# Optimization experiments

Hardware: AMD Instinct MI355X
Metric: run time of the kernel (lower is better)

Reference implementation:

```python
import jax, jax.numpy as jnp
import numpy as np

HK, DK, HV, DV = 16, 128, 32, 128
VE = (HV // HK) * DV  # 256
CHUNK = 64
KSZ = 4
EPS = 1e-12


def l2_normalize(x):
    sq = jnp.sum(x * x, axis=-1, keepdims=True)
    return x * jax.lax.rsqrt(sq + EPS)


def causal_dwconv_silu(x_bct, w, b):
    # x_bct: [B, C, T]; w: [C, 1, K]; b: [C]; causal depthwise conv then SiLU
    C = x_bct.shape[1]
    y = jax.lax.conv_general_dilated(
        x_bct, w, window_strides=(1,), padding=[(KSZ - 1, 0)],
        dimension_numbers=('NCH', 'OIH', 'NCH'), feature_group_count=C)
    return jax.nn.silu(y + b[None, :, None])


def setup_inputs() -> dict:
    key = jax.random.key(0)
    ks = jax.random.split(key, 12)
    B, T, H = 2, 2048, 2048
    s = 0.02
    return {
        'x': jax.random.normal(ks[0], (B, T, H), jnp.float32),
        'state': jnp.zeros((B, HK, DK, VE), jnp.float32),
        'Wq': jax.random.normal(ks[1], (HK * DK, H), jnp.float32) * s,
        'Wk': jax.random.normal(ks[2], (HK * DK, H), jnp.float32) * s,
        'Wv': jax.random.normal(ks[3], (HV * DV, H), jnp.float32) * s,
        'Wo': jax.random.normal(ks[4], (H, HV * DV), jnp.float32) * s,
        'Wa': jax.random.normal(ks[5], (HK, H), jnp.float32) * s,
        'Wb': jax.random.normal(ks[6], (HK, H), jnp.float32) * s,
        'qcW': jax.random.normal(ks[7], (HK * DK, 1, KSZ), jnp.float32) * 0.3,
        'qcB': jnp.zeros((HK * DK,), jnp.float32),
        'kcW': jax.random.normal(ks[8], (HK * DK, 1, KSZ), jnp.float32) * 0.3,
        'kcB': jnp.zeros((HK * DK,), jnp.float32),
        'vcW': jax.random.normal(ks[9], (HV * DV, 1, KSZ), jnp.float32) * 0.3,
        'vcB': jnp.zeros((HV * DV,), jnp.float32),
    }


def _forward(x, state, Wq, Wk, Wv, Wo, Wa, Wb, qcW, qcB, kcW, kcB, vcW, vcB):
    B, T, H = x.shape
    Cn = CHUNK
    # T is a multiple of CHUNK here (no padding needed)
    nc = T // Cn
    x_bct = jnp.transpose(x, (0, 2, 1))  # [B, H, T]
    # 1x1-conv projections == channelwise linear
    q = causal_dwconv_silu(jnp.einsum('qh,bht->bqt', Wq, x_bct), qcW, qcB)
    k = causal_dwconv_silu(jnp.einsum('qh,bht->bqt', Wk, x_bct), kcW, kcB)
    v = causal_dwconv_silu(jnp.einsum('vh,bht->bvt', Wv, x_bct), vcW, vcB)
    alpha = jax.nn.sigmoid(jnp.einsum('gh,bht->bgt', Wa, x_bct))  # [B,HK,T]
    beta = jax.nn.sigmoid(jnp.einsum('gh,bht->bgt', Wb, x_bct))

    q = jnp.transpose(q, (0, 2, 1)).reshape(B, T, HK, DK)
    k = jnp.transpose(k, (0, 2, 1)).reshape(B, T, HK, DK)
    # regroup value heads by key head: [B,T,HV,DV] -> [B,T,HK,VE]
    v = jnp.transpose(v, (0, 2, 1)).reshape(B, T, HK, VE)
    alpha = jnp.transpose(alpha, (0, 2, 1))  # [B,T,HK]
    beta = jnp.transpose(beta, (0, 2, 1))

    q = l2_normalize(q)
    k = l2_normalize(k)

    # time-major, chunked: [nc, Cn, B, HK, ...]
    def tmchunk(a):
        a = jnp.moveaxis(a, 1, 0)  # [T, B, ...]
        return a.reshape((nc, Cn) + a.shape[1:])

    qc, kc, vc, ac, bc = map(tmchunk, (q, k, v, alpha, beta))

    def step(s, inp):
        qt, kt, vt, at, bt = inp  # qt/kt [B,HK,DK], vt [B,HK,VE], at/bt [B,HK]
        s = s * at[..., None, None]
        retrieved = jnp.einsum('bhkv,bhk->bhv', s, kt)
        err = vt - retrieved
        s = s + bt[..., None, None] * (kt[..., :, None] * err[..., None, :])
        ot = jnp.einsum('bhkv,bhk->bhv', s, qt)
        return s, ot

    @jax.checkpoint
    def chunk_step(s, ch):
        return jax.lax.scan(step, s, ch)

    state, outs = jax.lax.scan(chunk_step, state, (qc, kc, vc, ac, bc))
    # outs: [nc, Cn, B, HK, VE] -> [B, T, HV*DV]
    out = outs.reshape(T, B, HK * VE)
    out = jnp.moveaxis(out, 0, 1)
    out = jnp.einsum('btv,ov->bto', out, Wo)
    return out, state


def reference(x, state, Wq, Wk, Wv, Wo, Wa, Wb, qcW, qcB, kcW, kcB, vcW, vcB):
    return _forward(x, state, Wq, Wk, Wv, Wo, Wa, Wb, qcW, qcB, kcW, kcB, vcW, vcB)
```

## Files before the change

kernel.cpp:

```cpp
#include <hip/hip_runtime.h>
#include <hip/hip_bf16.h>

typedef __attribute__((ext_vector_type(8))) __bf16 bf16x8;
typedef __attribute__((ext_vector_type(8))) short short8;
typedef __attribute__((ext_vector_type(4))) float floatx4;
using u16 = unsigned short;

#define GLOBAL_AS __attribute__((address_space(1)))
#define LDS_AS    __attribute__((address_space(3)))

__device__ __forceinline__ float b2f(u16 u) {
    union { unsigned int i; float f; } v; v.i = ((unsigned int)u) << 16; return v.f;
}
__device__ __forceinline__ u16 f2b(float f) {
    __hip_bfloat16 h = __float2bfloat16(f);
    return __builtin_bit_cast(u16, h);
}
__device__ __forceinline__ float ldf(const void* p, long i, bool isf32) {
    return isf32 ? ((const float*)p)[i] : b2f(((const u16*)p)[i]);
}
__device__ __forceinline__ void gload_lds16(const void* g, void* l) {
    __builtin_amdgcn_global_load_lds((const GLOBAL_AS unsigned int*)g,
                                     (LDS_AS unsigned int*)l, 16, 0, 0);
}
__device__ __forceinline__ float red8(float x) {
    int xi, yi;
    xi = __builtin_bit_cast(int, x);
    yi = __builtin_amdgcn_update_dpp(xi, xi, 0xB1, 0xF, 0xF, false);
    x += __builtin_bit_cast(float, yi);
    xi = __builtin_bit_cast(int, x);
    yi = __builtin_amdgcn_update_dpp(xi, xi, 0x4E, 0xF, 0xF, false);
    x += __builtin_bit_cast(float, yi);
    xi = __builtin_bit_cast(int, x);
    yi = __builtin_amdgcn_update_dpp(xi, xi, 0x141, 0xF, 0xF, false);
    x += __builtin_bit_cast(float, yi);
    return x;
}
__device__ __forceinline__ void unpack2(int d, float& lo, float& hi) {
    lo = __builtin_bit_cast(float, (int)((unsigned)d << 16));
    hi = __builtin_bit_cast(float, d & 0xffff0000);
}
__device__ __forceinline__ void unpack8(int4 d, float* f) {
    unpack2(d.x, f[0], f[1]); unpack2(d.y, f[2], f[3]);
    unpack2(d.z, f[4], f[5]); unpack2(d.w, f[6], f[7]);
}

__global__ void detect_dtype(const unsigned int* __restrict__ x, int* __restrict__ flag) {
    const int lane = threadIdx.x;
    int sane = 0;
    for (int i = lane; i < 256; i += 64) {
        const unsigned e = (x[i] >> 23) & 0xFF;
        sane += (e >= 100 && e <= 140) ? 1 : 0;
    }
#pragma unroll
    for (int m = 1; m < 64; m <<= 1) sane += __shfl_xor(sane, m, 64);
    if (lane == 0) *flag = (sane >= 128) ? 1 : 0;
}

__global__ __launch_bounds__(256) void cvt_bf16(
    const void* __restrict__ in, u16* __restrict__ out, long n, const int* __restrict__ flag) {
    const bool f32 = (*flag != 0);
    const long i = ((long)blockIdx.x * 256 + threadIdx.x) * 8;
    if (i >= n) return;
    if (f32) {
        const float* p = (const float*)in + i;
        floatx4 a = *(const floatx4*)p, b = *(const floatx4*)(p + 4);
        short8 o;
        o[0] = (short)f2b(a[0]); o[1] = (short)f2b(a[1]);
        o[2] = (short)f2b(a[2]); o[3] = (short)f2b(a[3]);
        o[4] = (short)f2b(b[0]); o[5] = (short)f2b(b[1]);
        o[6] = (short)f2b(b[2]); o[7] = (short)f2b(b[3]);
        *(short8*)(out + i) = o;
    } else {
        *(int4*)(out + i) = *(const int4*)((const u16*)in + i);
    }
}

__global__ __launch_bounds__(256) void gemm_bt128(
    const u16* __restrict__ A, const u16* __restrict__ B, void* __restrict__ C,
    int M, int N, int K, int cmode, const int* __restrict__ flag) {
    const bool c32 = (cmode == 1) || (cmode == 2 && *flag != 0);
    __shared__ __align__(16) u16 As[128 * 32];
    __shared__ __align__(16) u16 Bs[128 * 32];
    const int tid = threadIdx.x, lane = tid & 63, wave = tid >> 6;
    const int bm = blockIdx.y * 128, bn = blockIdx.x * 128;
    const int wm = (wave >> 1) * 64, wn = (wave & 1) * 64;
    const int fr = lane & 15, fq = lane >> 4;
    floatx4 acc[4][4] = {};

    const int srow = tid >> 2, scol = (tid & 3) * 8;
    const long abase = (long)(bm + srow) * K + scol;
    const long bbase = (long)(bn + srow) * K + scol;
    char* lA = (char*)As + (tid & ~63) * 16;
    char* lB = (char*)Bs + (tid & ~63) * 16;

    for (int k0 = 0; k0 < K; k0 += 32) {
        __syncthreads();
        gload_lds16(A + abase + k0, lA);
        gload_lds16(A + abase + (long)64 * K + k0, lA + 4096);
        gload_lds16(B + bbase + k0, lB);
        gload_lds16(B + bbase + (long)64 * K + k0, lB + 4096);
        __syncthreads();
        bf16x8 af[4], bf[4];
#pragma unroll
        for (int i = 0; i < 4; i++) {
            af[i] = __builtin_bit_cast(bf16x8, *(const short8*)&As[(wm + i * 16 + fr) * 32 + fq * 8]);
            bf[i] = __builtin_bit_cast(bf16x8, *(const short8*)&Bs[(wn + i * 16 + fr) * 32 + fq * 8]);
        }
#pragma unroll
        for (int mi = 0; mi < 4; mi++)
#pragma unroll
            for (int ni = 0; ni < 4; ni++)
                acc[mi][ni] = __builtin_amdgcn_mfma_f32_16x16x32_bf16(
                    af[mi], bf[ni], acc[mi][ni], 0, 0, 0);
    }
#pragma unroll
    for (int mi = 0; mi < 4; mi++)
#pragma unroll
        for (int ni = 0; ni < 4; ni++)
#pragma unroll
            for (int r = 0; r < 4; r++) {
                const int m = bm + wm + mi * 16 + fq * 4 + r;
                const int n = bn + wn + ni * 16 + fr;
                const float val = acc[mi][ni][r];
                const long ci = (long)m * N + n;
                if (c32) ((float*)C)[ci] = val;
                else ((u16*)C)[ci] = f2b(val);
            }
}

__global__ __launch_bounds__(256) void ab_gemm(
    const u16* __restrict__ xb, const u16* __restrict__ wab,
    float* __restrict__ alphaT, float* __restrict__ betaT) {
    __shared__ __align__(16) u16 As[64 * 64];
    __shared__ __align__(16) u16 Bs[32 * 64];
    const int tid = threadIdx.x, lane = tid & 63, wave = tid >> 6;
    const int bm = blockIdx.x * 64;
    const int fr = lane & 15, fq = lane >> 4;
    floatx4 acc[2] = {};

    const int srow = tid >> 3, scol = (tid & 7) * 8;
    char* lA = (char*)As + (tid & ~63) * 16;
    char* lB = (char*)Bs + (tid & ~63) * 16;

    for (int k0 = 0; k0 < 2048; k0 += 64) {
        __syncthreads();
        gload_lds16(xb + (long)(bm + srow) * 2048 + k0 + scol, lA);
        gload_lds16(xb + (long)(bm + 32 + srow) * 2048 + k0 + scol, lA + 4096);
        gload_lds16(wab + (long)srow * 2048 + k0 + scol, lB);
        __syncthreads();
#pragma unroll
        for (int ks = 0; ks < 2; ks++) {
            bf16x8 af = __builtin_bit_cast(bf16x8,
                *(const short8*)&As[(wave * 16 + fr) * 64 + ks * 32 + fq * 8]);
#pragma unroll
            for (int nt = 0; nt < 2; nt++) {
                bf16x8 bf = __builtin_bit_cast(bf16x8,
                    *(const short8*)&Bs[(nt * 16 + fr) * 64 + ks * 32 + fq * 8]);
                acc[nt] = __builtin_amdgcn_mfma_f32_16x16x32_bf16(af, bf, acc[nt], 0, 0, 0);
            }
        }
    }
#pragma unroll
    for (int nt = 0; nt < 2; nt++)
#pragma unroll
        for (int r = 0; r < 4; r++) {
            const int m = bm + wave * 16 + fq * 4 + r;
            const int n = nt * 16 + fr;
            const int b = m >> 11, t = m & 2047;
            const float s = 1.f / (1.f + __expf(-acc[nt][r]));
            if (n < 16) alphaT[((long)b * 16 + n) * 2048 + t] = s;
            else betaT[((long)b * 16 + (n - 16)) * 2048 + t] = s;
        }
}

__global__ __launch_bounds__(256) void conv_silu_norm(
    const u16* __restrict__ pre, const void* __restrict__ cw,
    const void* __restrict__ cb, u16* __restrict__ out, const int* __restrict__ flag) {
    const bool f32 = (*flag != 0);
    const int bt = blockIdx.x;
    const int t = bt & 2047;
    const int tid = threadIdx.x;
    const int c0 = tid * 8;
    float y[8];
    float ss = 0.f;
#pragma unroll
    for (int j = 0; j < 8; j++) {
        const int c = c0 + j;
        float acc = ldf(cb, c, f32);
#pragma unroll
        for (int i = 0; i < 4; i++) {
            if (t - 3 + i >= 0)
                acc += ldf(cw, c * 4 + i, f32) * b2f(pre[(long)(bt - 3 + i) * 2048 + c]);
        }
        const float s = acc / (1.f + __expf(-acc));
        y[j] = s;
        ss += s * s;
    }
#pragma unroll
    for (int m = 1; m < 16; m <<= 1) ss += __shfl_xor(ss, m, 64);
    const float inv = rsqrtf(ss + 1e-12f);
#pragma unroll
    for (int j = 0; j < 8; j++) out[(long)bt * 2048 + c0 + j] = f2b(y[j] * inv);
}

__global__ __launch_bounds__(256) void conv_silu_v(
    const u16* __restrict__ pre, const void* __restrict__ cw,
    const void* __restrict__ cb, u16* __restrict__ out, const int* __restrict__ flag) {
    const bool f32 = (*flag != 0);
    const int bt = blockIdx.x;
    const int t = bt & 2047;
    const int tid = threadIdx.x;
    const int c0 = tid * 16;
#pragma unroll
    for (int j = 0; j < 16; j++) {
        const int c = c0 + j;
        float acc = ldf(cb, c, f32);
#pragma unroll
        for (int i = 0; i < 4; i++) {
            if (t - 3 + i >= 0)
                acc += ldf(cw, c * 4 + i, f32) * b2f(pre[(long)(bt - 3 + i) * 4096 + c]);
        }
        out[(long)bt * 4096 + c] = f2b(acc / (1.f + __expf(-acc)));
    }
}

__global__ __launch_bounds__(256) void recurrence_kernel(
    const u16* __restrict__ qn, const u16* __restrict__ kn,
    const u16* __restrict__ vn, const float* __restrict__ alphaT,
    const float* __restrict__ betaT, const void* __restrict__ state_in,
    u16* __restrict__ outs, void* __restrict__ d_out, const int* __restrict__ flag) {
    const bool f32 = (*flag != 0);
    const int blk = blockIdx.x;
    const int vb = blk & 7, h = (blk >> 3) & 15, b = blk >> 7;
    const int tid = threadIdx.x, lane = tid & 63, wave = tid >> 6;
    const int kg = lane & 7, vq = lane >> 3;
    const int vloc = wave * 8 + vq;
    const int vglob = vb * 32 + vloc;

    float S[16];
    const long stbase = ((long)(b * 16 + h) * 128 + kg * 16) * 256 + vglob;
#pragma unroll
    for (int j = 0; j < 16; j++) S[j] = ldf(state_in, stbase + (long)j * 256, f32);

    __shared__ __align__(16) u16 kbuf[16 * 128];
    __shared__ __align__(16) u16 qbuf[16 * 128];
    __shared__ __align__(16) u16 vbuf[16 * 32];

    const long abase = (long)(b * 16 + h) * 2048;
    const int srow = tid >> 4, scol = (tid & 15) * 8;
    char* lK = (char*)kbuf + (tid & ~63) * 16;
    char* lQ = (char*)qbuf + (tid & ~63) * 16;

    for (int c = 0; c < 128; ++c) {
        const int t0 = c * 16;
        const float aw = alphaT[abase + t0 + (lane & 15)];
        const float bw = betaT[abase + t0 + (lane & 15)];
        __syncthreads();
        const long gkq = ((long)b * 2048 + t0 + srow) * 2048 + h * 128 + scol;
        gload_lds16(kn + gkq, lK);
        gload_lds16(qn + gkq, lQ);
        if (tid < 64) {
            const long gv = ((long)b * 2048 + t0 + (lane >> 2)) * 4096 + h * 256 + vb * 32 + (lane & 3) * 8;
            gload_lds16(vn + gv, (char*)vbuf);
        }
        __syncthreads();

        int4 kA = *(const int4*)(kbuf + kg * 16);
        int4 kB = *(const int4*)(kbuf + kg * 16 + 8);
        int4 qA = *(const int4*)(qbuf + kg * 16);
        int4 qB = *(const int4*)(qbuf + kg * 16 + 8);
        u16 vcur = vbuf[vloc];

#pragma unroll
        for (int tt = 0; tt < 16; ++tt) {
            int4 kA_n, kB_n, qA_n, qB_n;
            u16 v_n;
            if (tt < 15) {
                kA_n = *(const int4*)(kbuf + (tt + 1) * 128 + kg * 16);
                kB_n = *(const int4*)(kbuf + (tt + 1) * 128 + kg * 16 + 8);
                qA_n = *(const int4*)(qbuf + (tt + 1) * 128 + kg * 16);
                qB_n = *(const int4*)(qbuf + (tt + 1) * 128 + kg * 16 + 8);
                v_n  = vbuf[(tt + 1) * 32 + vloc];
            }
            const float a = __builtin_bit_cast(float,
                __builtin_amdgcn_readlane(__builtin_bit_cast(int, aw), tt));
            const float bb = __builtin_bit_cast(float,
                __builtin_amdgcn_readlane(__builtin_bit_cast(int, bw), tt));
            float kf[16], qf[16];
            unpack8(kA, kf);
            unpack8(kB, kf + 8);
            unpack8(qA, qf);
            unpack8(qB, qf + 8);
            float r0 = 0.f, r1 = 0.f;
#pragma unroll
            for (int j = 0; j < 8; j++) {
                r0 = fmaf(S[j], kf[j], r0);
                r1 = fmaf(S[8 + j], kf[8 + j], r1);
            }
            float r = red8(r0 + r1);
            const float vv = b2f(vcur);
            const float err = fmaf(-a, r, vv);
            const float cc = bb * err;
            float o0 = 0.f, o1 = 0.f;
#pragma unroll
            for (int j = 0; j < 8; j++) {
                S[j] = fmaf(cc, kf[j], a * S[j]);
                S[8 + j] = fmaf(cc, kf[8 + j], a * S[8 + j]);
                o0 = fmaf(S[j], qf[j], o0);
                o1 = fmaf(S[8 + j], qf[8 + j], o1);
            }
            const float o = red8(o0 + o1);
            if (kg == 0)
                outs[((long)b * 2048 + t0 + tt) * 4096 + h * 256 + vglob] = f2b(o);
            if (tt < 15) { kA = kA_n; kB = kB_n; qA = qA_n; qB = qB_n; vcur = v_n; }
        }
    }
#pragma unroll
    for (int j = 0; j < 16; j++) {
        const long idx = 8388608L + stbase + (long)j * 256;
        if (f32) ((float*)d_out)[idx] = S[j];
        else ((u16*)d_out)[idx] = f2b(S[j]);
    }
}

extern "C" void kernel_launch(void* const* d_in, const int* in_sizes, int n_in,
                              void* d_out, int out_size, void* d_ws, size_t ws_size,
                              hipStream_t stream) {
    const void* x   = d_in[0];
    const void* st0 = d_in[1];
    const void* Wq  = d_in[2];
    const void* Wk  = d_in[3];
    const void* Wv  = d_in[4];
    const void* Wo  = d_in[5];
    const void* Wa  = d_in[6];
    const void* Wb  = d_in[7];
    const void* qcW = d_in[8];
    const void* qcB = d_in[9];
    const void* kcW = d_in[10];
    const void* kcB = d_in[11];
    const void* vcW = d_in[12];
    const void* vcB = d_in[13];

    const int M = 4096;
    const long MB = 1024L * 1024L;
    char* w = (char*)d_ws;
    int*   flag   = (int*)w;
    float* alphaT = (float*)(w + 1024);
    float* betaT  = (float*)(w + 1024 + 262144);
    u16*   wab    = (u16*)(w + 1024 + 524288);
    u16* xb    = (u16*)(w + 1 * MB);
    u16* wqb   = (u16*)(w + 17 * MB);
    u16* wkb   = (u16*)(w + 25 * MB);
    u16* wvb   = (u16*)(w + 33 * MB);
    u16* qpreb = (u16*)(w + 49 * MB);
    u16* kpreb = (u16*)(w + 65 * MB);
    u16* vpreb = (u16*)(w + 81 * MB);
    u16* qn    = (u16*)(w + 113 * MB);
    u16* kn    = (u16*)(w + 129 * MB);
    u16* vn    = (u16*)(w + 145 * MB);
    u16* wob   = xb;
    u16* outs  = qpreb;

    dim3 blk(256);
    detect_dtype<<<dim3(1), dim3(64), 0, stream>>>((const unsigned int*)x, flag);

    cvt_bf16<<<dim3(4096), blk, 0, stream>>>(x,  xb,  8388608L, flag);
    cvt_bf16<<<dim3(2048), blk, 0, stream>>>(Wq, wqb, 4194304L, flag);
    cvt_bf16<<<dim3(2048), blk, 0, stream>>>(Wk, wkb, 4194304L, flag);
    cvt_bf16<<<dim3(4096), blk, 0, stream>>>(Wv, wvb, 8388608L, flag);
    cvt_bf16<<<dim3(16),   blk, 0, stream>>>(Wa, wab, 32768L, flag);
    cvt_bf16<<<dim3(16),   blk, 0, stream>>>(Wb, wab + 32768, 32768L, flag);

    gemm_bt128<<<dim3(2048 / 128, M / 128), blk, 0, stream>>>(xb, wqb, qpreb, M, 2048, 2048, 3, flag);
    gemm_bt128<<<dim3(2048 / 128, M / 128), blk, 0, stream>>>(xb, wkb, kpreb, M, 2048, 2048, 3, flag);
    gemm_bt128<<<dim3(4096 / 128, M / 128), blk, 0, stream>>>(xb, wvb, vpreb, M, 4096, 2048, 3, flag);
    ab_gemm<<<dim3(64), blk, 0, stream>>>(xb, wab, alphaT, betaT);

    cvt_bf16<<<dim3(4096), blk, 0, stream>>>(Wo, wob, 8388608L, flag);

    conv_silu_norm<<<dim3(M), blk, 0, stream>>>(qpreb, qcW, qcB, qn, flag);
    conv_silu_norm<<<dim3(M), blk, 0, stream>>>(kpreb, kcW, kcB, kn, flag);
    conv_silu_v<<<dim3(M), blk, 0, stream>>>(vpreb, vcW, vcB, vn, flag);

    recurrence_kernel<<<dim3(256), blk, 0, stream>>>(qn, kn, vn, alphaT, betaT, st0,
                                                     outs, d_out, flag);

    gemm_bt128<<<dim3(2048 / 128, M / 128), blk, 0, stream>>>(outs, wob, d_out, M, 2048, 4096, 2, flag);
}
```

Baseline: 1.816 ms.

## Double-buffer recurrence inputs in LDS as pre-converted fp32 with register prefetch

The recurrence kernel now loads the next chunk's k/q/v/alpha/beta into registers while the current chunk is being computed. It then writes them to a double-buffered LDS area already converted to fp32, in an interleaved layout so each lane reads conflict-free float4 vectors. This removes one barrier per chunk, hides global load latency behind compute, and takes the bf16 unpack out of the serial inner loop. The cost is four times the LDS footprint and extra registers for the prefetched data, which may lower occupancy.

After: 1.706 ms. -6.1%, faster.

```diff
diff --git a/kernel.cpp b/kernel.cpp
--- a/kernel.cpp
+++ b/kernel.cpp
@@ -243,79 +243,117 @@
 #pragma unroll
     for (int j = 0; j < 16; j++) S[j] = ldf(state_in, stbase + (long)j * 256, f32);
 
-    __shared__ __align__(16) u16 kbuf[16 * 128];
-    __shared__ __align__(16) u16 qbuf[16 * 128];
-    __shared__ __align__(16) u16 vbuf[16 * 32];
-
+    __shared__ __align__(16) float kf[2][16 * 128];
+    __shared__ __align__(16) float qf[2][16 * 128];
+    __shared__ __align__(16) float vf[2][16 * 32];
+
+    const int srow = tid >> 4, sc8 = (tid & 15) * 8, vc2 = (tid & 15) * 2;
+    const long gkq0 = ((long)b * 2048 + srow) * 2048 + h * 128 + sc8;
+    const long gv0  = ((long)b * 2048 + srow) * 4096 + h * 256 + vb * 32 + vc2;
     const long abase = (long)(b * 16 + h) * 2048;
-    const int srow = tid >> 4, scol = (tid & 15) * 8;
-    char* lK = (char*)kbuf + (tid & ~63) * 16;
-    char* lQ = (char*)qbuf + (tid & ~63) * 16;
+
+    int4 gk, gq;
+    unsigned int gv;
+    float ga, gb;
+
+    auto stage_write = [&](int buf) {
+        const int kgg = sc8 >> 4, i0 = (sc8 >> 2) & 3;
+        float fk[8], fq_[8];
+        unpack8(gk, fk);
+        unpack8(gq, fq_);
+        const int base = srow * 128 + kgg * 4;
+        *(floatx4*)&kf[buf][base + i0 * 32]       = floatx4{fk[0], fk[1], fk[2], fk[3]};
+        *(floatx4*)&kf[buf][base + (i0 + 1) * 32] = floatx4{fk[4], fk[5], fk[6], fk[7]};
+        *(floatx4*)&qf[buf][base + i0 * 32]       = floatx4{fq_[0], fq_[1], fq_[2], fq_[3]};
+        *(floatx4*)&qf[buf][base + (i0 + 1) * 32] = floatx4{fq_[4], fq_[5], fq_[6], fq_[7]};
+        vf[buf][srow * 32 + vc2]     = b2f((u16)(gv & 0xffffu));
+        vf[buf][srow * 32 + vc2 + 1] = b2f((u16)(gv >> 16));
+    };
+
+    gk = *(const int4*)(kn + gkq0);
+    gq = *(const int4*)(qn + gkq0);
+    gv = *(const unsigned int*)(vn + gv0);
+    ga = alphaT[abase + (lane & 15)];
+    gb = betaT[abase + (lane & 15)];
+    stage_write(0);
+    __syncthreads();
 
     for (int c = 0; c < 128; ++c) {
-        const int t0 = c * 16;
-        const float aw = alphaT[abase + t0 + (lane & 15)];
-        const float bw = betaT[abase + t0 + (lane & 15)];
-        __syncthreads();
-        const long gkq = ((long)b * 2048 + t0 + srow) * 2048 + h * 128 + scol;
-        gload_lds16(kn + gkq, lK);
-        gload_lds16(qn + gkq, lQ);
-        if (tid < 64) {
-            const long gv = ((long)b * 2048 + t0 + (lane >> 2)) * 4096 + h * 256 + vb * 32 + (lane & 3) * 8;
-            gload_lds16(vn + gv, (char*)vbuf);
-        }
-        __syncthreads();
-
-        int4 kA = *(const int4*)(kbuf + kg * 16);
-        int4 kB = *(const int4*)(kbuf + kg * 16 + 8);
-        int4 qA = *(const int4*)(qbuf + kg * 16);
-        int4 qB = *(const int4*)(qbuf + kg * 16 + 8);
-        u16 vcur = vbuf[vloc];
+        const int cur = c & 1;
+        const float aw = ga, bw = gb;
+        if (c + 1 < 128) {
+            const long off = (long)(c + 1) * 16 * 2048;
+            gk = *(const int4*)(kn + gkq0 + off);
+            gq = *(const int4*)(qn + gkq0 + off);
+            gv = *(const unsigned int*)(vn + gv0 + (long)(c + 1) * 16 * 4096);
+            ga = alphaT[abase + (c + 1) * 16 + (lane & 15)];
+            gb = betaT[abase + (c + 1) * 16 + (lane & 15)];
+        }
+
+        const float* kfp = kf[cur];
+        const float* qfp = qf[cur];
+        const float* vfp = vf[cur];
+
+        floatx4 ka[4], qa[4];
+#pragma unroll
+        for (int i = 0; i < 4; i++) {
+            ka[i] = *(const floatx4*)&kfp[i * 32 + kg * 4];
+            qa[i] = *(const floatx4*)&qfp[i * 32 + kg * 4];
+        }
+        float vcur = vfp[vloc];
 
 #pragma unroll
         for (int tt = 0; tt < 16; ++tt) {
-            int4 kA_n, kB_n, qA_n, qB_n;
-            u16 v_n;
+            floatx4 ka_n[4], qa_n[4];
+            float v_n = 0.f;
             if (tt < 15) {
-                kA_n = *(const int4*)(kbuf + (tt + 1) * 128 + kg * 16);
-                kB_n = *(const int4*)(kbuf + (tt + 1) * 128 + kg * 16 + 8);
-                qA_n = *(const int4*)(qbuf + (tt + 1) * 128 + kg * 16);
-                qB_n = *(const int4*)(qbuf + (tt + 1) * 128 + kg * 16 + 8);
-                v_n  = vbuf[(tt + 1) * 32 + vloc];
+#pragma unroll
+                for (int i = 0; i < 4; i++) {
+                    ka_n[i] = *(const floatx4*)&kfp[(tt + 1) * 128 + i * 32 + kg * 4];
+                    qa_n[i] = *(const floatx4*)&qfp[(tt + 1) * 128 + i * 32 + kg * 4];
+                }
+                v_n = vfp[(tt + 1) * 32 + vloc];
             }
             const float a = __builtin_bit_cast(float,
                 __builtin_amdgcn_readlane(__builtin_bit_cast(int, aw), tt));
             const float bb = __builtin_bit_cast(float,
                 __builtin_amdgcn_readlane(__builtin_bit_cast(int, bw), tt));
-            float kf[16], qf[16];
-            unpack8(kA, kf);
-            unpack8(kB, kf + 8);
-            unpack8(qA, qf);
-            unpack8(qB, qf + 8);
             float r0 = 0.f, r1 = 0.f;
 #pragma unroll
-            for (int j = 0; j < 8; j++) {
-                r0 = fmaf(S[j], kf[j], r0);
-                r1 = fmaf(S[8 + j], kf[8 + j], r1);
-            }
-            float r = red8(r0 + r1);
-            const float vv = b2f(vcur);
-            const float err = fmaf(-a, r, vv);
+            for (int i = 0; i < 4; i++)
+#pragma unroll
+                for (int j = 0; j < 4; j++) {
+                    const int idx = i * 4 + j;
+                    if (idx < 8) r0 = fmaf(S[idx], ka[i][j], r0);
+                    else         r1 = fmaf(S[idx], ka[i][j], r1);
+                }
+            const float r = red8(r0 + r1);
+            const float err = fmaf(-a, r, vcur);
             const float cc = bb * err;
             float o0 = 0.f, o1 = 0.f;
 #pragma unroll
-            for (int j = 0; j < 8; j++) {
-                S[j] = fmaf(cc, kf[j], a * S[j]);
-                S[8 + j] = fmaf(cc, kf[8 + j], a * S[8 + j]);
-                o0 = fmaf(S[j], qf[j], o0);
-                o1 = fmaf(S[8 + j], qf[8 + j], o1);
-            }
+            for (int i = 0; i < 4; i++)
+#pragma unroll
+                for (int j = 0; j < 4; j++) {
+                    const int idx = i * 4 + j;
+                    S[idx] = fmaf(cc, ka[i][j], a * S[idx]);
+                    if (idx < 8) o0 = fmaf(S[idx], qa[i][j], o0);
+                    else         o1 = fmaf(S[idx], qa[i][j], o1);
+                }
             const float o = red8(o0 + o1);
             if (kg == 0)
-                outs[((long)b * 2048 + t0 + tt) * 4096 + h * 256 + vglob] = f2b(o);
-            if (tt < 15) { kA = kA_n; kB = kB_n; qA = qA_n; qB = qB_n; vcur = v_n; }
-        }
-    }
+                outs[((long)b * 2048 + c * 16 + tt) * 4096 + h * 256 + vglob] = f2b(o);
+            if (tt < 15) {
+#pragma unroll
+                for (int i = 0; i < 4; i++) { ka[i] = ka_n[i]; qa[i] = qa_n[i]; }
+                vcur = v_n;
+            }
+        }
+
+        if (c + 1 < 128) stage_write(cur ^ 1);
+        __syncthreads();
+    }
+
 #pragma unroll
     for (int j = 0; j < 16; j++) {
         const long idx = 8388608L + stbase + (long)j * 256;
```
